# Optimization experiments

Hardware: AMD Instinct MI355X
Metric: run time of the kernel (lower is better)

Reference implementation:

```python
import jax, jax.numpy as jnp
import numpy as np

B, S, D, H = 2, 2048, 2048, 16
HD = D // H  # head_dim = 128
THETA = 10000.0


def _rope(x, sin, cos):
    # x: [b,h,s,hd]; rotate-half convention: cat(-x2, x1)
    d = x.shape[-1] // 2
    x1, x2 = x[..., :d], x[..., d:]
    x_rot = jnp.concatenate([-x2, x1], axis=-1)
    return x * cos + x_rot * sin


def setup_inputs() -> dict:
    key = jax.random.key(0)
    k0, k1, k2 = jax.random.split(key, 3)
    x = jax.random.normal(k0, (B, S, D), jnp.float32)
    Wqkv = jax.random.normal(k1, (D, 3 * D), jnp.float32) * 0.02
    Wproj = jax.random.normal(k2, (D, D), jnp.float32) * 0.02
    # causal mask [1,1,S,S]
    mask = jnp.tril(jnp.ones((S, S), jnp.int32))[None, None]
    # rotary tables [1,1,S,HD]
    inv_freq = 1.0 / (THETA ** (np.arange(0, HD, 2, dtype=np.float64) / HD))
    freqs = np.outer(np.arange(S, dtype=np.float64), inv_freq)
    emb = np.concatenate([freqs, freqs], axis=-1)
    sin = jnp.asarray(np.sin(emb), jnp.float32)[None, None]
    cos = jnp.asarray(np.cos(emb), jnp.float32)[None, None]
    return {"x": x, "mask": mask, "sin": sin, "cos": cos, "Wqkv": Wqkv, "Wproj": Wproj}


def reference(x, mask, sin, cos, Wqkv, Wproj):
    b, s, d = x.shape
    qkv = (x @ Wqkv).reshape(b, s, 3, H, HD).transpose(2, 0, 3, 1, 4)  # [3,b,h,s,hd]
    q, k, v = qkv[0], qkv[1], qkv[2]
    q = _rope(q, sin[:, :, :s, :], cos[:, :, :s, :])
    k = _rope(k, sin[:, :, :s, :], cos[:, :, :s, :])
    att = jnp.einsum('bhqd,bhkd->bhqk', q, k) / jnp.sqrt(jnp.float32(HD))
    att = jnp.where(mask == 0, -jnp.inf, att)
    probs = jax.nn.softmax(att, axis=-1)
    out = jnp.einsum('bhqk,bhkd->bhqd', probs, v)
    out = out.transpose(0, 2, 1, 3).reshape(b, s, d)
    return out @ Wproj
```

## Files before the change

### kernel.cpp

```cpp
#include <hip/hip_runtime.h>
#include <hip/hip_bf16.h>
#include <stdint.h>

#define B_ 2
#define S_ 2048
#define D_ 2048
#define H_ 16
#define HD_ 128
#define N3_ 6144

typedef __attribute__((ext_vector_type(8))) short short8;
typedef __attribute__((ext_vector_type(4))) float f32x4;
typedef __hip_bfloat16 bf16;

__global__ void cast_bf16_kernel(const float* __restrict__ in, bf16* __restrict__ out, int n4) {
  int i = blockIdx.x * blockDim.x + threadIdx.x;
  if (i >= n4) return;
  float4 v = ((const float4*)in)[i];
  bf16 a = __float2bfloat16(v.x), b = __float2bfloat16(v.y);
  bf16 c = __float2bfloat16(v.z), d = __float2bfloat16(v.w);
  ushort4 o;
  o.x = *(unsigned short*)&a; o.y = *(unsigned short*)&b;
  o.z = *(unsigned short*)&c; o.w = *(unsigned short*)&d;
  ((ushort4*)out)[i] = o;
}

__global__ void transpose_cast_kernel(const float* __restrict__ in, bf16* __restrict__ out,
                                      int R, int C) {
  __shared__ float tile[32][33];
  int c0 = blockIdx.x * 32, r0 = blockIdx.y * 32;
  int tx = threadIdx.x, ty = threadIdx.y;
#pragma unroll
  for (int i = 0; i < 4; i++)
    tile[ty + i * 8][tx] = in[(size_t)(r0 + ty + i * 8) * C + c0 + tx];
  __syncthreads();
#pragma unroll
  for (int i = 0; i < 4; i++) {
    int oc = ty + i * 8;
    out[(size_t)(c0 + oc) * R + r0 + tx] = __float2bfloat16(tile[tx][oc]);
  }
}

__device__ __forceinline__ void store_c(float* p, float v) { *p = v; }
__device__ __forceinline__ void store_c(bf16* p, float v) { *p = __float2bfloat16(v); }

template <typename CT>
__global__ __launch_bounds__(256, 2) void gemm_bt_kernel(
    const bf16* __restrict__ A, const bf16* __restrict__ Bt, CT* __restrict__ C,
    int M, int N, int K) {
  __shared__ bf16 a_lds[128 * 64];
  __shared__ bf16 b_lds[128 * 64];
  int t = threadIdx.x;
  int lane = t & 63, w = t >> 6;
  int lane15 = lane & 15, quad = lane >> 4;
  int wm = w >> 1, wn = w & 1;
  int m0 = blockIdx.y * 128, n0 = blockIdx.x * 128;

  f32x4 acc[4][4];
#pragma unroll
  for (int i = 0; i < 4; i++)
#pragma unroll
    for (int j = 0; j < 4; j++) acc[i][j] = (f32x4){0.f, 0.f, 0.f, 0.f};

  const bf16* ga = A + (size_t)m0 * K;
  const bf16* gb = Bt + (size_t)n0 * K;

  int sr[4], sgc[4];
#pragma unroll
  for (int i = 0; i < 4; i++) {
    int ch = t + i * 256;
    sr[i] = ch >> 3;
    sgc[i] = (ch & 7) ^ (sr[i] & 7);
  }
  int sx = lane15 & 7;

  for (int kt = 0; kt < K; kt += 64) {
    __syncthreads();
#pragma unroll
    for (int i = 0; i < 4; i++) {
      int ch = t + i * 256;
      __builtin_amdgcn_global_load_lds(
          (const __attribute__((address_space(1))) void*)(ga + (size_t)sr[i] * K + kt + sgc[i] * 8),
          (__attribute__((address_space(3))) void*)(a_lds + ch * 8), 16, 0, 0);
      __builtin_amdgcn_global_load_lds(
          (const __attribute__((address_space(1))) void*)(gb + (size_t)sr[i] * K + kt + sgc[i] * 8),
          (__attribute__((address_space(3))) void*)(b_lds + ch * 8), 16, 0, 0);
    }
    __syncthreads();

#pragma unroll
    for (int ks = 0; ks < 2; ks++) {
      int slot = (ks * 4 + quad) ^ sx;
      short8 af[4], bfr[4];
#pragma unroll
      for (int mt = 0; mt < 4; mt++)
        af[mt] = *(const short8*)(a_lds + (wm * 64 + mt * 16 + lane15) * 64 + slot * 8);
#pragma unroll
      for (int nt = 0; nt < 4; nt++)
        bfr[nt] = *(const short8*)(b_lds + (wn * 64 + nt * 16 + lane15) * 64 + slot * 8);
#pragma unroll
      for (int mt = 0; mt < 4; mt++)
#pragma unroll
        for (int nt = 0; nt < 4; nt++)
          acc[mt][nt] = __builtin_amdgcn_mfma_f32_16x16x32_bf16(af[mt], bfr[nt], acc[mt][nt], 0, 0, 0);
    }
  }

#pragma unroll
  for (int mt = 0; mt < 4; mt++)
#pragma unroll
    for (int nt = 0; nt < 4; nt++)
#pragma unroll
      for (int r = 0; r < 4; r++) {
        int row = m0 + wm * 64 + mt * 16 + quad * 4 + r;
        int col = n0 + wn * 64 + nt * 16 + lane15;
        store_c(&C[(size_t)row * N + col], acc[mt][nt][r]);
      }
}

__global__ void rope_qk_kernel(const bf16* __restrict__ qkv, const float* __restrict__ sinp,
                               const float* __restrict__ cosp, bf16* __restrict__ Q,
                               bf16* __restrict__ K) {
  int bs = blockIdx.x;
  int b = bs >> 11, s = bs & 2047;
  const bf16* row = qkv + (size_t)bs * N3_;
  for (int p = threadIdx.x; p < 2048; p += 256) {
    int g = p >> 10;
    int pp = p & 1023;
    int h = pp >> 6, i = pp & 63;
    float x1 = __bfloat162float(row[g * D_ + h * HD_ + i]);
    float x2 = __bfloat162float(row[g * D_ + h * HD_ + i + 64]);
    float sn = sinp[s * HD_ + i];
    float cs = cosp[s * HD_ + i];
    float o1 = x1 * cs - x2 * sn;
    float o2 = x2 * cs + x1 * sn;
    bf16* dst = (g == 0) ? Q : K;
    size_t base = (((size_t)b * H_ + h) * S_ + s) * HD_;
    dst[base + i] = __float2bfloat16(o1);
    dst[base + i + 64] = __float2bfloat16(o2);
  }
}

__global__ void transpose_v_kernel(const bf16* __restrict__ qkv, bf16* __restrict__ Vt) {
  __shared__ __align__(16) bf16 tile[64][HD_ + 8];
  int bh = blockIdx.y;
  int b = bh >> 4, h = bh & 15;
  int s0 = blockIdx.x * 64;
  int t = threadIdx.x;
#pragma unroll
  for (int i = 0; i < 4; i++) {
    int ch = t + i * 256;
    int r = ch >> 4, cc = (ch & 15) * 8;
    *(uint4*)&tile[r][cc] =
        *(const uint4*)(qkv + (size_t)(b * S_ + s0 + r) * N3_ + 2 * D_ + h * HD_ + cc);
  }
  __syncthreads();
#pragma unroll
  for (int i = 0; i < 4; i++) {
    int ch = t + i * 256;
    int hd = ch >> 3, sl = (ch & 7) * 8;
    union { bf16 v[8]; uint4 u; } tmp;
#pragma unroll
    for (int j = 0; j < 8; j++) tmp.v[j] = tile[sl + j][hd];
    *(uint4*)(Vt + (((size_t)b * H_ + h) * HD_ + hd) * S_ + s0 + sl) = tmp.u;
  }
}

__global__ __launch_bounds__(256, 2) void attn_kernel(
    const bf16* __restrict__ Q, const bf16* __restrict__ K, const bf16* __restrict__ Vt,
    bf16* __restrict__ Out) {
  __shared__ __align__(16) bf16 k_lds[64 * HD_];
  __shared__ __align__(16) bf16 v_lds[HD_ * 64];
  __shared__ __align__(16) bf16 p_lds[4][32][64 + 8];
  const float SCALE_LOG2 = 0.08838834764831845f * 1.4426950408889634f;

  int bh = blockIdx.x;
  int b = bh >> 4, h = bh & 15;
  int qi = (S_ / 128 - 1) - blockIdx.y;
  int q0 = qi * 128;
  int t = threadIdx.x, w = t >> 6, lane = t & 63;
  int lane15 = lane & 15, quad = lane >> 4;

  const bf16* Qb = Q + ((size_t)b * H_ + h) * S_ * HD_;
  const bf16* Kb = K + ((size_t)b * H_ + h) * S_ * HD_;
  const bf16* Vb = Vt + ((size_t)b * H_ + h) * HD_ * S_;

  short8 qf[2][4];
#pragma unroll
  for (int mt = 0; mt < 2; mt++) {
    int qrow = q0 + w * 32 + mt * 16 + lane15;
#pragma unroll
    for (int k0 = 0; k0 < 4; k0++)
      qf[mt][k0] = *(const short8*)(Qb + (size_t)qrow * HD_ + k0 * 32 + quad * 8);
  }

  f32x4 o_acc[2][8];
#pragma unroll
  for (int mt = 0; mt < 2; mt++)
#pragma unroll
    for (int i = 0; i < 8; i++) o_acc[mt][i] = (f32x4){0.f, 0.f, 0.f, 0.f};
  float m_run[2][4], l_run[2][4];
#pragma unroll
  for (int mt = 0; mt < 2; mt++)
#pragma unroll
    for (int r = 0; r < 4; r++) { m_run[mt][r] = -1e30f; l_run[mt][r] = 0.f; }
  int row_base[2];
  row_base[0] = q0 + w * 32 + quad * 4;
  row_base[1] = q0 + w * 32 + 16 + quad * 4;

  int tmax = 2 * qi + 1;

  int kr[4], kgc[4], vr[4], vgc[4];
#pragma unroll
  for (int i = 0; i < 4; i++) {
    int ch = t + i * 256;
    kr[i] = ch >> 4; kgc[i] = (ch & 15) ^ (kr[i] & 15);
    vr[i] = ch >> 3; vgc[i] = (ch & 7) ^ (vr[i] & 7);
  }

  for (int tkv = 0; tkv <= tmax; tkv++) {
    int kv0 = tkv * 64;
    __syncthreads();
#pragma unroll
    for (int i = 0; i < 4; i++) {
      int ch = t + i * 256;
      __builtin_amdgcn_global_load_lds(
          (const __attribute__((address_space(1))) void*)(Kb + (size_t)(kv0 + kr[i]) * HD_ + kgc[i] * 8),
          (__attribute__((address_space(3))) void*)(k_lds + ch * 8), 16, 0, 0);
      __builtin_amdgcn_global_load_lds(
          (const __attribute__((address_space(1))) void*)(Vb + (size_t)vr[i] * S_ + kv0 + vgc[i] * 8),
          (__attribute__((address_space(3))) void*)(v_lds + ch * 8), 16, 0, 0);
    }
    __syncthreads();

    bool masked = (tkv >= 2 * qi);

#pragma unroll
    for (int mt = 0; mt < 2; mt++) {
      f32x4 s_acc[4];
#pragma unroll
      for (int nt = 0; nt < 4; nt++) {
        f32x4 acc = (f32x4){0.f, 0.f, 0.f, 0.f};
#pragma unroll
        for (int k0 = 0; k0 < 4; k0++) {
          int r2 = nt * 16 + lane15;
          int cch = (k0 * 4 + quad) ^ (r2 & 15);
          short8 kf = *(const short8*)(k_lds + r2 * HD_ + cch * 8);
          acc = __builtin_amdgcn_mfma_f32_16x16x32_bf16(qf[mt][k0], kf, acc, 0, 0, 0);
        }
        s_acc[nt] = acc;
      }

      float p[4][4];
      float rowmax[4] = {-1e30f, -1e30f, -1e30f, -1e30f};
#pragma unroll
      for (int nt = 0; nt < 4; nt++) {
        int col = kv0 + nt * 16 + lane15;
#pragma unroll
        for (int r = 0; r < 4; r++) {
          float v = s_acc[nt][r] * SCALE_LOG2;
          if (masked && col > row_base[mt] + r) v = -1e30f;
          p[nt][r] = v;
          rowmax[r] = fmaxf(rowmax[r], v);
        }
      }
      float alpha[4];
#pragma unroll
      for (int r = 0; r < 4; r++) {
        float v = rowmax[r];
        v = fmaxf(v, __shfl_xor(v, 1));
        v = fmaxf(v, __shfl_xor(v, 2));
        v = fmaxf(v, __shfl_xor(v, 4));
        v = fmaxf(v, __shfl_xor(v, 8));
        float mnew = fmaxf(m_run[mt][r], v);
        alpha[r] = __builtin_amdgcn_exp2f(m_run[mt][r] - mnew);
        m_run[mt][r] = mnew;
      }
#pragma unroll
      for (int r = 0; r < 4; r++) {
        float lsum = 0.f;
#pragma unroll
        for (int nt = 0; nt < 4; nt++) {
          float e = __builtin_amdgcn_exp2f(p[nt][r] - m_run[mt][r]);
          p[nt][r] = e;
          lsum += e;
        }
        l_run[mt][r] = l_run[mt][r] * alpha[r] + lsum;
      }
#pragma unroll
      for (int on = 0; on < 8; on++) {
        f32x4 o = o_acc[mt][on];
        o[0] *= alpha[0]; o[1] *= alpha[1]; o[2] *= alpha[2]; o[3] *= alpha[3];
        o_acc[mt][on] = o;
      }
#pragma unroll
      for (int nt = 0; nt < 4; nt++)
#pragma unroll
        for (int r = 0; r < 4; r++)
          p_lds[w][mt * 16 + quad * 4 + r][nt * 16 + lane15] = __float2bfloat16(p[nt][r]);
    }

#pragma unroll
    for (int mt = 0; mt < 2; mt++)
#pragma unroll
      for (int k0 = 0; k0 < 2; k0++) {
        short8 pf = *(const short8*)&p_lds[w][mt * 16 + lane15][k0 * 32 + quad * 8];
#pragma unroll
        for (int on = 0; on < 8; on++) {
          int rv = on * 16 + lane15;
          int cch = (k0 * 4 + quad) ^ (rv & 7);
          short8 vf = *(const short8*)(v_lds + rv * 64 + cch * 8);
          o_acc[mt][on] = __builtin_amdgcn_mfma_f32_16x16x32_bf16(pf, vf, o_acc[mt][on], 0, 0, 0);
        }
      }
  }

#pragma unroll
  for (int mt = 0; mt < 2; mt++) {
#pragma unroll
    for (int r = 0; r < 4; r++) {
      float v = l_run[mt][r];
      v += __shfl_xor(v, 1);
      v += __shfl_xor(v, 2);
      v += __shfl_xor(v, 4);
      v += __shfl_xor(v, 8);
      l_run[mt][r] = 1.f / v;
    }
#pragma unroll
    for (int on = 0; on < 8; on++)
#pragma unroll
      for (int r = 0; r < 4; r++) {
        int s = row_base[mt] + r;
        Out[((size_t)(b * S_ + s)) * D_ + h * HD_ + on * 16 + lane15] =
            __float2bfloat16(o_acc[mt][on][r] * l_run[mt][r]);
      }
  }
}

extern "C" void kernel_launch(void* const* d_in, const int* in_sizes, int n_in,
                              void* d_out, int out_size, void* d_ws, size_t ws_size,
                              hipStream_t stream) {
  const float* x = (const float*)d_in[0];
  const float* sinp = (const float*)d_in[2];
  const float* cosp = (const float*)d_in[3];
  const float* Wqkv = (const float*)d_in[4];
  const float* Wproj = (const float*)d_in[5];
  float* out = (float*)d_out;

  char* ws = (char*)d_ws;
  bf16* x_bf = (bf16*)ws;    ws += (size_t)B_ * S_ * D_ * 2;
  bf16* wqkv_t = (bf16*)ws;  ws += (size_t)N3_ * D_ * 2;
  bf16* wproj_t = (bf16*)ws; ws += (size_t)D_ * D_ * 2;
  bf16* qkv = (bf16*)ws;     ws += (size_t)B_ * S_ * N3_ * 2;
  bf16* Qp = (bf16*)ws;      ws += (size_t)B_ * S_ * D_ * 2;
  bf16* Kp = (bf16*)ws;      ws += (size_t)B_ * S_ * D_ * 2;
  bf16* Vt = (bf16*)ws;      ws += (size_t)B_ * S_ * D_ * 2;
  bf16* attn = (bf16*)ws;    ws += (size_t)B_ * S_ * D_ * 2;

  int nx4 = B_ * S_ * D_ / 4;
  cast_bf16_kernel<<<nx4 / 256, 256, 0, stream>>>(x, x_bf, nx4);
  transpose_cast_kernel<<<dim3(N3_ / 32, D_ / 32), dim3(32, 8), 0, stream>>>(Wqkv, wqkv_t, D_, N3_);
  transpose_cast_kernel<<<dim3(D_ / 32, D_ / 32), dim3(32, 8), 0, stream>>>(Wproj, wproj_t, D_, D_);

  gemm_bt_kernel<bf16><<<dim3(N3_ / 128, (B_ * S_) / 128), 256, 0, stream>>>(
      x_bf, wqkv_t, qkv, B_ * S_, N3_, D_);

  rope_qk_kernel<<<B_ * S_, 256, 0, stream>>>(qkv, sinp, cosp, Qp, Kp);
  transpose_v_kernel<<<dim3(S_ / 64, B_ * H_), 256, 0, stream>>>(qkv, Vt);

  attn_kernel<<<dim3(B_ * H_, S_ / 128), 256, 0, stream>>>(Qp, Kp, Vt, attn);

  gemm_bt_kernel<float><<<dim3(D_ / 128, (B_ * S_) / 128), 256, 0, stream>>>(
      attn, wproj_t, out, B_ * S_, D_, D_);
}
```

Measured before the change: 432.8 us.

## Double-buffer KV tiles and pair causal query blocks per workgroup

The attention kernel now keeps two LDS buffers for K and V and prefetches the next tile with global_load_lds while computing on the current one, using vmcnt waits and raw barriers in place of full syncthreads. Each workgroup processes two query blocks, qi and 15-qi, so that causal work is balanced across workgroups, and the grid is halved. Launch bounds drop to one block per CU minimum, which allows more registers but gives fewer resident workgroups. Only 256 workgroups remain, so occupancy on the GPU falls, and the hand-written waitcnt encodings must be correct for this target.

```diff
diff --git a/kernel.cpp b/kernel.cpp
--- a/kernel.cpp
+++ b/kernel.cpp
@@ -166,18 +166,16 @@
   }
 }
 
-__global__ __launch_bounds__(256, 2) void attn_kernel(
+__global__ __launch_bounds__(256, 1) void attn_kernel(
     const bf16* __restrict__ Q, const bf16* __restrict__ K, const bf16* __restrict__ Vt,
     bf16* __restrict__ Out) {
-  __shared__ __align__(16) bf16 k_lds[64 * HD_];
-  __shared__ __align__(16) bf16 v_lds[HD_ * 64];
+  __shared__ __align__(16) bf16 k_lds[2][64 * HD_];
+  __shared__ __align__(16) bf16 v_lds[2][HD_ * 64];
   __shared__ __align__(16) bf16 p_lds[4][32][64 + 8];
   const float SCALE_LOG2 = 0.08838834764831845f * 1.4426950408889634f;
 
   int bh = blockIdx.x;
   int b = bh >> 4, h = bh & 15;
-  int qi = (S_ / 128 - 1) - blockIdx.y;
-  int q0 = qi * 128;
   int t = threadIdx.x, w = t >> 6, lane = t & 63;
   int lane15 = lane & 15, quad = lane >> 4;
 
@@ -185,31 +183,6 @@
   const bf16* Kb = K + ((size_t)b * H_ + h) * S_ * HD_;
   const bf16* Vb = Vt + ((size_t)b * H_ + h) * HD_ * S_;
 
-  short8 qf[2][4];
-#pragma unroll
-  for (int mt = 0; mt < 2; mt++) {
-    int qrow = q0 + w * 32 + mt * 16 + lane15;
-#pragma unroll
-    for (int k0 = 0; k0 < 4; k0++)
-      qf[mt][k0] = *(const short8*)(Qb + (size_t)qrow * HD_ + k0 * 32 + quad * 8);
-  }
-
-  f32x4 o_acc[2][8];
-#pragma unroll
-  for (int mt = 0; mt < 2; mt++)
-#pragma unroll
-    for (int i = 0; i < 8; i++) o_acc[mt][i] = (f32x4){0.f, 0.f, 0.f, 0.f};
-  float m_run[2][4], l_run[2][4];
-#pragma unroll
-  for (int mt = 0; mt < 2; mt++)
-#pragma unroll
-    for (int r = 0; r < 4; r++) { m_run[mt][r] = -1e30f; l_run[mt][r] = 0.f; }
-  int row_base[2];
-  row_base[0] = q0 + w * 32 + quad * 4;
-  row_base[1] = q0 + w * 32 + 16 + quad * 4;
-
-  int tmax = 2 * qi + 1;
-
   int kr[4], kgc[4], vr[4], vgc[4];
 #pragma unroll
   for (int i = 0; i < 4; i++) {
@@ -218,122 +191,168 @@
     vr[i] = ch >> 3; vgc[i] = (ch & 7) ^ (vr[i] & 7);
   }
 
-  for (int tkv = 0; tkv <= tmax; tkv++) {
-    int kv0 = tkv * 64;
-    __syncthreads();
+  auto issue_kv = [&](int kv0, int bufi) {
 #pragma unroll
     for (int i = 0; i < 4; i++) {
       int ch = t + i * 256;
       __builtin_amdgcn_global_load_lds(
           (const __attribute__((address_space(1))) void*)(Kb + (size_t)(kv0 + kr[i]) * HD_ + kgc[i] * 8),
-          (__attribute__((address_space(3))) void*)(k_lds + ch * 8), 16, 0, 0);
+          (__attribute__((address_space(3))) void*)(&k_lds[bufi][ch * 8]), 16, 0, 0);
       __builtin_amdgcn_global_load_lds(
           (const __attribute__((address_space(1))) void*)(Vb + (size_t)vr[i] * S_ + kv0 + vgc[i] * 8),
-          (__attribute__((address_space(3))) void*)(v_lds + ch * 8), 16, 0, 0);
-    }
-    __syncthreads();
-
-    bool masked = (tkv >= 2 * qi);
-
+          (__attribute__((address_space(3))) void*)(&v_lds[bufi][ch * 8]), 16, 0, 0);
+    }
+  };
+
+#pragma unroll 1
+  for (int ph = 0; ph < 2; ph++) {
+    int qi = ph ? (15 - (int)blockIdx.y) : (int)blockIdx.y;
+    int q0 = qi * 128;
+    int ntiles = 2 * qi + 2;
+
+    short8 qf[2][4];
 #pragma unroll
     for (int mt = 0; mt < 2; mt++) {
-      f32x4 s_acc[4];
-#pragma unroll
-      for (int nt = 0; nt < 4; nt++) {
-        f32x4 acc = (f32x4){0.f, 0.f, 0.f, 0.f};
-#pragma unroll
-        for (int k0 = 0; k0 < 4; k0++) {
-          int r2 = nt * 16 + lane15;
-          int cch = (k0 * 4 + quad) ^ (r2 & 15);
-          short8 kf = *(const short8*)(k_lds + r2 * HD_ + cch * 8);
-          acc = __builtin_amdgcn_mfma_f32_16x16x32_bf16(qf[mt][k0], kf, acc, 0, 0, 0);
-        }
-        s_acc[nt] = acc;
+      int qrow = q0 + w * 32 + mt * 16 + lane15;
+#pragma unroll
+      for (int k0 = 0; k0 < 4; k0++)
+        qf[mt][k0] = *(const short8*)(Qb + (size_t)qrow * HD_ + k0 * 32 + quad * 8);
+    }
+
+    f32x4 o_acc[2][8];
+#pragma unroll
+    for (int mt = 0; mt < 2; mt++)
+#pragma unroll
+      for (int i = 0; i < 8; i++) o_acc[mt][i] = (f32x4){0.f, 0.f, 0.f, 0.f};
+    float m_run[2][4], l_run[2][4];
+#pragma unroll
+    for (int mt = 0; mt < 2; mt++)
+#pragma unroll
+      for (int r = 0; r < 4; r++) { m_run[mt][r] = -1e30f; l_run[mt][r] = 0.f; }
+    int row_base[2];
+    row_base[0] = q0 + w * 32 + quad * 4;
+    row_base[1] = q0 + w * 32 + 16 + quad * 4;
+
+    issue_kv(0, 0);
+
+#pragma unroll 1
+    for (int tk = 0; tk < ntiles; tk++) {
+      int cur = tk & 1;
+      int kv0 = tk * 64;
+      if (tk + 1 < ntiles) {
+        issue_kv(kv0 + 64, cur ^ 1);
+        __builtin_amdgcn_s_waitcnt(0xF78);
+      } else {
+        __builtin_amdgcn_s_waitcnt(0xF70);
       }
-
-      float p[4][4];
-      float rowmax[4] = {-1e30f, -1e30f, -1e30f, -1e30f};
-#pragma unroll
-      for (int nt = 0; nt < 4; nt++) {
-        int col = kv0 + nt * 16 + lane15;
+      __builtin_amdgcn_s_barrier();
+
+      const bf16* kb = k_lds[cur];
+      const bf16* vb = v_lds[cur];
+      bool masked = (tk >= 2 * qi);
+
+#pragma unroll
+      for (int mt = 0; mt < 2; mt++) {
+        f32x4 s_acc[4];
+#pragma unroll
+        for (int nt = 0; nt < 4; nt++) {
+          f32x4 acc = (f32x4){0.f, 0.f, 0.f, 0.f};
+#pragma unroll
+          for (int k0 = 0; k0 < 4; k0++) {
+            int r2 = nt * 16 + lane15;
+            int cch = (k0 * 4 + quad) ^ (r2 & 15);
+            short8 kf = *(const short8*)(kb + r2 * HD_ + cch * 8);
+            acc = __builtin_amdgcn_mfma_f32_16x16x32_bf16(qf[mt][k0], kf, acc, 0, 0, 0);
+          }
+          s_acc[nt] = acc;
+        }
+
+        float p[4][4];
+        float rowmax[4] = {-1e30f, -1e30f, -1e30f, -1e30f};
+#pragma unroll
+        for (int nt = 0; nt < 4; nt++) {
+          int col = kv0 + nt * 16 + lane15;
+#pragma unroll
+          for (int r = 0; r < 4; r++) {
+            float v = s_acc[nt][r] * SCALE_LOG2;
+            if (masked && col > row_base[mt] + r) v = -1e30f;
+            p[nt][r] = v;
+            rowmax[r] = fmaxf(rowmax[r], v);
+          }
+        }
+        float alpha[4];
 #pragma unroll
         for (int r = 0; r < 4; r++) {
-          float v = s_acc[nt][r] * SCALE_LOG2;
-          if (masked && col > row_base[mt] + r) v = -1e30f;
-          p[nt][r] = v;
-          rowmax[r] = fmaxf(rowmax[r], v);
-        }
+          float v = rowmax[r];
+          v = fmaxf(v, __shfl_xor(v, 1));
+          v = fmaxf(v, __shfl_xor(v, 2));
+          v = fmaxf(v, __shfl_xor(v, 4));
+          v = fmaxf(v, __shfl_xor(v, 8));
+          float mnew = fmaxf(m_run[mt][r], v);
+          alpha[r] = __builtin_amdgcn_exp2f(m_run[mt][r] - mnew);
+          m_run[mt][r] = mnew;
+        }
+#pragma unroll
+        for (int r = 0; r < 4; r++) {
+          float lsum = 0.f;
+#pragma unroll
+          for (int nt = 0; nt < 4; nt++) {
+            float e = __builtin_amdgcn_exp2f(p[nt][r] - m_run[mt][r]);
+            p[nt][r] = e;
+            lsum += e;
+          }
+          l_run[mt][r] = l_run[mt][r] * alpha[r] + lsum;
+        }
+#pragma unroll
+        for (int on = 0; on < 8; on++) {
+          f32x4 o = o_acc[mt][on];
+          o[0] *= alpha[0]; o[1] *= alpha[1]; o[2] *= alpha[2]; o[3] *= alpha[3];
+          o_acc[mt][on] = o;
+        }
+#pragma unroll
+        for (int nt = 0; nt < 4; nt++)
+#pragma unroll
+          for (int r = 0; r < 4; r++)
+            p_lds[w][mt * 16 + quad * 4 + r][nt * 16 + lane15] = __float2bfloat16(p[nt][r]);
       }
-      float alpha[4];
+
+#pragma unroll
+      for (int mt = 0; mt < 2; mt++)
+#pragma unroll
+        for (int k0 = 0; k0 < 2; k0++) {
+          short8 pf = *(const short8*)&p_lds[w][mt * 16 + lane15][k0 * 32 + quad * 8];
+#pragma unroll
+          for (int on = 0; on < 8; on++) {
+            int rv = on * 16 + lane15;
+            int cch = (k0 * 4 + quad) ^ (rv & 7);
+            short8 vf = *(const short8*)(v_lds[cur] + rv * 64 + cch * 8);
+            o_acc[mt][on] = __builtin_amdgcn_mfma_f32_16x16x32_bf16(pf, vf, o_acc[mt][on], 0, 0, 0);
+          }
+        }
+
+      __builtin_amdgcn_s_barrier();
+    }
+
+#pragma unroll
+    for (int mt = 0; mt < 2; mt++) {
 #pragma unroll
       for (int r = 0; r < 4; r++) {
-        float v = rowmax[r];
-        v = fmaxf(v, __shfl_xor(v, 1));
-        v = fmaxf(v, __shfl_xor(v, 2));
-        v = fmaxf(v, __shfl_xor(v, 4));
-        v = fmaxf(v, __shfl_xor(v, 8));
-        float mnew = fmaxf(m_run[mt][r], v);
-        alpha[r] = __builtin_amdgcn_exp2f(m_run[mt][r] - mnew);
-        m_run[mt][r] = mnew;
+        float v = l_run[mt][r];
+        v += __shfl_xor(v, 1);
+        v += __shfl_xor(v, 2);
+        v += __shfl_xor(v, 4);
+        v += __shfl_xor(v, 8);
+        l_run[mt][r] = 1.f / v;
       }
 #pragma unroll
-      for (int r = 0; r < 4; r++) {
-        float lsum = 0.f;
-#pragma unroll
-        for (int nt = 0; nt < 4; nt++) {
-          float e = __builtin_amdgcn_exp2f(p[nt][r] - m_run[mt][r]);
-          p[nt][r] = e;
-          lsum += e;
-        }
-        l_run[mt][r] = l_run[mt][r] * alpha[r] + lsum;
-      }
-#pragma unroll
-      for (int on = 0; on < 8; on++) {
-        f32x4 o = o_acc[mt][on];
-        o[0] *= alpha[0]; o[1] *= alpha[1]; o[2] *= alpha[2]; o[3] *= alpha[3];
-        o_acc[mt][on] = o;
-      }
-#pragma unroll
-      for (int nt = 0; nt < 4; nt++)
-#pragma unroll
-        for (int r = 0; r < 4; r++)
-          p_lds[w][mt * 16 + quad * 4 + r][nt * 16 + lane15] = __float2bfloat16(p[nt][r]);
-    }
-
-#pragma unroll
-    for (int mt = 0; mt < 2; mt++)
-#pragma unroll
-      for (int k0 = 0; k0 < 2; k0++) {
-        short8 pf = *(const short8*)&p_lds[w][mt * 16 + lane15][k0 * 32 + quad * 8];
-#pragma unroll
-        for (int on = 0; on < 8; on++) {
-          int rv = on * 16 + lane15;
-          int cch = (k0 * 4 + quad) ^ (rv & 7);
-          short8 vf = *(const short8*)(v_lds + rv * 64 + cch * 8);
-          o_acc[mt][on] = __builtin_amdgcn_mfma_f32_16x16x32_bf16(pf, vf, o_acc[mt][on], 0, 0, 0);
-        }
-      }
-  }
-
-#pragma unroll
-  for (int mt = 0; mt < 2; mt++) {
-#pragma unroll
-    for (int r = 0; r < 4; r++) {
-      float v = l_run[mt][r];
-      v += __shfl_xor(v, 1);
-      v += __shfl_xor(v, 2);
-      v += __shfl_xor(v, 4);
-      v += __shfl_xor(v, 8);
-      l_run[mt][r] = 1.f / v;
-    }
-#pragma unroll
-    for (int on = 0; on < 8; on++)
-#pragma unroll
-      for (int r = 0; r < 4; r++) {
-        int s = row_base[mt] + r;
-        Out[((size_t)(b * S_ + s)) * D_ + h * HD_ + on * 16 + lane15] =
-            __float2bfloat16(o_acc[mt][on][r] * l_run[mt][r]);
-      }
+      for (int on = 0; on < 8; on++)
+#pragma unroll
+        for (int r = 0; r < 4; r++) {
+          int s = row_base[mt] + r;
+          Out[((size_t)(b * S_ + s)) * D_ + h * HD_ + on * 16 + lane15] =
+              __float2bfloat16(o_acc[mt][on][r] * l_run[mt][r]);
+        }
+    }
   }
 }
 
@@ -368,7 +387,7 @@
   rope_qk_kernel<<<B_ * S_, 256, 0, stream>>>(qkv, sinp, cosp, Qp, Kp);
   transpose_v_kernel<<<dim3(S_ / 64, B_ * H_), 256, 0, stream>>>(qkv, Vt);
 
-  attn_kernel<<<dim3(B_ * H_, S_ / 128), 256, 0, stream>>>(Qp, Kp, Vt, attn);
+  attn_kernel<<<dim3(B_ * H_, S_ / 128 / 2), 256, 0, stream>>>(Qp, Kp, Vt, attn);
 
   gemm_bt_kernel<float><<<dim3(D_ / 128, (B_ * S_) / 128), 256, 0, stream>>>(
       attn, wproj_t, out, B_ * S_, D_, D_);
```

Result: no change. 434.1 us (+0.3%).
